# Optimization experiments

Measured on AMD Instinct MI355X. Metric: run time of the kernel, lower is better.

The kernel has to match this reference:

```python
import jax, jax.numpy as jnp
import numpy as np

BS, N, HID, INPUT, PREK, KHOP = 16, 1024, 64, 64, 4, 3
D = 2 * HID            # hidden channel dim (128)
F = 2 * INPUT          # input feature dim (128)
C = F + D              # graphconv input channels (256)
NM = KHOP + 1          # num_metrics = k_hop*n_supports + 1 with n_supports=1
PI = 3.141592653589793
EMB_RANGE = (12.0 + 2.0) / HID   # (gamma + epsilon) / hidden_size


def setup_inputs() -> dict:
    key = jax.random.key(0)
    ks = jax.random.split(key, 12)
    inputs = jax.random.normal(ks[0], (BS, N, F), jnp.float32)
    # per-sample dynamic support; scale by 1/N to keep Chebyshev recursion stable
    supports = jax.random.uniform(ks[1], (BS, N, N), jnp.float32) / N
    hidden_states = jax.random.normal(ks[2], (BS, PREK, N, D), jnp.float32)
    W = jax.random.normal(ks[3], (D, D), jnp.float32) * 0.02
    b = jax.random.normal(ks[4], (N, D), jnp.float32) * 0.02
    R = jax.random.normal(ks[5], (PREK, N, HID), jnp.float32) * 0.02
    gc_w = jax.random.normal(ks[6], (D, C * NM), jnp.float32) * 0.02
    gc_b = jax.random.normal(ks[7], (D,), jnp.float32) * 0.02
    ev_att_w = jax.random.normal(ks[8], (1, N * D), jnp.float32) * 0.001
    ev_att_b = jax.random.normal(ks[9], (1,), jnp.float32) * 0.02
    att_w = jax.random.normal(ks[10], (1, N * D), jnp.float32) * 0.001
    att_b = jax.random.normal(ks[11], (1,), jnp.float32) * 0.02
    return {"inputs": inputs, "supports": supports, "hidden_states": hidden_states,
            "W": W, "b": b, "R": R, "gc_w": gc_w, "gc_b": gc_b,
            "ev_att_w": ev_att_w, "ev_att_b": ev_att_b,
            "att_w": att_w, "att_b": att_b}


def reference(inputs, supports, hidden_states, W, b, R, gc_w, gc_b,
              ev_att_w, ev_att_b, att_w, att_b):
    bs, k, n, d = hidden_states.shape
    # split inputs / last hidden into real/imag halves
    re_in, im_in = jnp.split(inputs, 2, axis=-1)          # [bs,n,INPUT]
    preH = hidden_states[:, -1]                           # [bs,n,d]
    re_p, im_p = jnp.split(preH, 2, axis=-1)              # [bs,n,HID]
    conv_in = jnp.concatenate([re_in, re_p, im_in, im_p], axis=-1)  # [bs,n,C]

    # diffusion graph conv (Chebyshev-style recursion over single batched support)
    x0 = conv_in
    x1 = jnp.matmul(supports, x0)                         # [bs,n,C]
    xs = [x0, x1]
    for _ in range(2, KHOP + 1):
        x2 = 2.0 * jnp.matmul(supports, x1) - x0
        xs.append(x2)
        x0, x1 = x1, x2
    # stack K metrics, permute to [bs,n,C,K], flatten (channel-major, step-minor)
    x = jnp.stack(xs, axis=0).transpose(1, 2, 3, 0).reshape(bs, n, C * NM)
    gco = x @ gc_w.T + gc_b                               # [bs,n,d]

    # EvolutionCell attention over g=1 group (kept for faithfulness)
    xe = gco.reshape(bs, 1, n * d)
    se = xe @ ev_att_w.T + ev_att_b                       # [bs,1,1]
    we = jax.nn.softmax(se, axis=1)
    conv_out = (xe * we).sum(axis=1).reshape(bs, n, d)

    # leaky_relu_ (slope 0.01)
    conv_out = jnp.where(conv_out >= 0, conv_out, 0.01 * conv_out)

    # RotatE-style complex phase rotation of hidden states
    phase = R / (EMB_RANGE / PI)                          # [k,n,HID]
    re_rel, im_rel = jnp.cos(phase), jnp.sin(phase)
    re_h, im_h = jnp.split(hidden_states, 2, axis=-1)     # [bs,k,n,HID]
    re_new = re_rel * re_h - im_rel * im_h
    im_new = im_rel * re_h + re_rel * im_h
    new_states = jnp.concatenate([re_new, im_new], axis=-1)  # [bs,k,n,d]

    # attention over k memory slots
    xa = new_states.reshape(bs, k, n * d)
    sa = xa @ att_w.T + att_b                             # [bs,k,1]
    wa = jax.nn.softmax(sa, axis=1)
    att = (xa * wa).sum(axis=1).reshape(bs, n, d)

    output = conv_out @ W + b[None] + att                 # [bs,n,d]
    new_hidden = jnp.concatenate([hidden_states[:, 1:], output[:, None]], axis=1)
    return output, new_hidden
```

## Files before the change

### kernel.cpp

```cpp
#include <hip/hip_runtime.h>
#include <cstddef>

constexpr float PHASE_SCALE = (float)(3.141592653589793 / ((12.0 + 2.0) / 64.0));

typedef __bf16 bf16;
typedef __bf16 bf16x4 __attribute__((ext_vector_type(4)));
typedef __bf16 bf16x8 __attribute__((ext_vector_type(8)));
typedef float floatx4 __attribute__((ext_vector_type(4)));

__global__ __launch_bounds__(256) void prep_kernel(
    const float4* __restrict__ S, bf16* __restrict__ Sbf,
    const float* __restrict__ R,
    const float* __restrict__ gcw, const float* __restrict__ W,
    bf16* __restrict__ gtAll, bf16* __restrict__ WT,
    const float* __restrict__ inp, const float* __restrict__ hs,
    bf16* __restrict__ xAll, bf16* __restrict__ xT0,
    const float* __restrict__ attw, float* __restrict__ part)
{
    __shared__ bf16 tile[64][65];
    __shared__ float red[256];
    const int bid = blockIdx.x;
    const int tid = threadIdx.x;

    if (bid < 8192) {
        int gi = bid * 256 + tid;
        #pragma unroll
        for (int it = 0; it < 2; ++it) {
            int idx = gi + it * 2097152;
            float4 v = S[idx];
            bf16x4 o;
            o[0] = (bf16)v.x; o[1] = (bf16)v.y; o[2] = (bf16)v.z; o[3] = (bf16)v.w;
            *(bf16x4*)(Sbf + (size_t)idx * 4) = o;
        }
    } else if (bid < 9216) {
        int bid2 = bid - 8192;
        int b = bid2 >> 6;
        int by = (bid2 >> 2) & 15;
        int bx = bid2 & 3;
        int n0 = by * 64, c0 = bx * 64;
        #pragma unroll
        for (int it = 0; it < 16; ++it) {
            int idx = it * 256 + tid;
            int cl = idx & 63, nl = idx >> 6;
            int n = n0 + nl, c = c0 + cl;
            const float* irow = inp + ((size_t)b * 1024 + n) * 128;
            const float* prow = hs + (((size_t)b * 4 + 3) * 1024 + n) * 128;
            float v;
            if (c < 64)       v = irow[c];
            else if (c < 128) v = prow[c - 64];
            else if (c < 192) v = irow[c - 64];
            else              v = prow[c - 128];
            bf16 vb = (bf16)v;
            xAll[((size_t)b * 1024 + n) * 1024 + c] = vb;
            tile[nl][cl] = vb;
        }
        __syncthreads();
        #pragma unroll
        for (int it = 0; it < 16; ++it) {
            int idx = it * 256 + tid;
            int nl = idx & 63, cl = idx >> 6;
            xT0[((size_t)b * 256 + c0 + cl) * 1024 + n0 + nl] = tile[nl][cl];
        }
    } else if (bid < 9728) {
        int bid3 = bid - 9216;
        int bk = bid3 & 63;
        int k = bk & 3;
        int chunk = bid3 >> 6;
        const float* hbase = hs + (size_t)bk * 131072;
        float acc = 0.f;
        for (int idx = tid; idx < 2048; idx += 256) {
            int h4 = (idx & 15) * 4;
            int n = chunk * 128 + (idx >> 4);
            float4 rr  = *(const float4*)(R + (size_t)k * 65536 + n * 64 + h4);
            float4 re  = *(const float4*)(hbase + (size_t)n * 128 + h4);
            float4 im  = *(const float4*)(hbase + (size_t)n * 128 + 64 + h4);
            float4 wre = *(const float4*)(attw + (size_t)n * 128 + h4);
            float4 wim = *(const float4*)(attw + (size_t)n * 128 + 64 + h4);
            float sv, cv;
            __sincosf(rr.x * PHASE_SCALE, &sv, &cv);
            acc += (cv * re.x - sv * im.x) * wre.x + (sv * re.x + cv * im.x) * wim.x;
            __sincosf(rr.y * PHASE_SCALE, &sv, &cv);
            acc += (cv * re.y - sv * im.y) * wre.y + (sv * re.y + cv * im.y) * wim.y;
            __sincosf(rr.z * PHASE_SCALE, &sv, &cv);
            acc += (cv * re.z - sv * im.z) * wre.z + (sv * re.z + cv * im.z) * wim.z;
            __sincosf(rr.w * PHASE_SCALE, &sv, &cv);
            acc += (cv * re.w - sv * im.w) * wre.w + (sv * re.w + cv * im.w) * wim.w;
        }
        red[tid] = acc;
        __syncthreads();
        for (int s2 = 128; s2 > 0; s2 >>= 1) {
            if (tid < s2) red[tid] += red[tid + s2];
            __syncthreads();
        }
        if (tid == 0) part[bk * 8 + chunk] = red[0];
    } else {
        int gi = (bid - 9728) * 256 + tid;
        if (gi < 131072) {
            int d = gi >> 10;
            int m = (gi >> 8) & 3;
            int c = gi & 255;
            gtAll[gi] = (bf16)gcw[(size_t)d * 1024 + c * 4 + m];
        } else {
            int r = gi - 131072;
            int n = r >> 7, k = r & 127;
            WT[r] = (bf16)W[(size_t)k * 128 + n];
        }
    }
}

__global__ __launch_bounds__(256) void cheb_mfma_kernel(
    const bf16* __restrict__ S, const bf16* __restrict__ xT,
    const bf16* __restrict__ xTprev, bf16* __restrict__ outT,
    bf16* __restrict__ xAll, int mslot, float alpha)
{
    __shared__ bf16 ldsA[64 * 64];
    __shared__ bf16 ldsB[128 * 64];
    const int f = blockIdx.x;
    const int b = (f & 7) + 8 * ((f >> 3) & 1);
    const int t = f >> 4;
    const int c0 = (t & 1) * 128;
    const int n0 = (t >> 1) * 64;
    const int tid = threadIdx.x;
    const int wave = tid >> 6, lane = tid & 63;
    const int wr = (wave >> 1) * 32, wc = (wave & 1) * 64;
    const int l15 = lane & 15, quad = lane >> 4;

    const bf16* Sb = S + (size_t)b * 1048576;
    const bf16* xb = xT + (size_t)b * 262144;

    const int lrow = lane >> 3;
    const int segsw = (lane & 7) ^ lrow;

    floatx4 acc[2][4] = {};

    for (int k0 = 0; k0 < 1024; k0 += 64) {
        #pragma unroll
        for (int u = 0; u < 2; ++u) {
            int Rr = wave * 16 + u * 8;
            const bf16* gp = Sb + (size_t)(n0 + Rr + lrow) * 1024 + k0 + segsw * 8;
            __builtin_amdgcn_global_load_lds(
                (const __attribute__((address_space(1))) void*)gp,
                (__attribute__((address_space(3))) void*)(ldsA + Rr * 64), 16, 0, 0);
        }
        #pragma unroll
        for (int v = 0; v < 4; ++v) {
            int Cq = wave * 32 + v * 8;
            const bf16* gp = xb + (size_t)(c0 + Cq + lrow) * 1024 + k0 + segsw * 8;
            __builtin_amdgcn_global_load_lds(
                (const __attribute__((address_space(1))) void*)gp,
                (__attribute__((address_space(3))) void*)(ldsB + Cq * 64), 16, 0, 0);
        }
        __syncthreads();
        #pragma unroll
        for (int ks = 0; ks < 2; ++ks) {
            bf16x8 af[2], bfr[4];
            #pragma unroll
            for (int i = 0; i < 2; ++i) {
                int row = wr + i * 16 + l15;
                int slot = (ks * 4 + quad) ^ (row & 7);
                af[i] = *(const bf16x8*)(ldsA + row * 64 + slot * 8);
            }
            #pragma unroll
            for (int j = 0; j < 4; ++j) {
                int col = wc + j * 16 + l15;
                int slot = (ks * 4 + quad) ^ (col & 7);
                bfr[j] = *(const bf16x8*)(ldsB + col * 64 + slot * 8);
            }
            #pragma unroll
            for (int i = 0; i < 2; ++i)
                #pragma unroll
                for (int j = 0; j < 4; ++j)
                    acc[i][j] = __builtin_amdgcn_mfma_f32_16x16x32_bf16(af[i], bfr[j], acc[i][j], 0, 0, 0);
        }
        __syncthreads();
    }

    const bf16* pT = xTprev ? xTprev + (size_t)b * 262144 : nullptr;
    bf16* oT = outT ? outT + (size_t)b * 262144 : nullptr;
    bf16* xr = xAll + (size_t)b * 1048576 + mslot * 256;
    #pragma unroll
    for (int i = 0; i < 2; ++i) {
        int nb = n0 + wr + i * 16 + quad * 4;
        #pragma unroll
        for (int j = 0; j < 4; ++j) {
            int cg = c0 + wc + j * 16 + l15;
            float v[4];
            #pragma unroll
            for (int r = 0; r < 4; ++r) v[r] = alpha * acc[i][j][r];
            if (pT) {
                const bf16* pp = pT + (size_t)cg * 1024 + nb;
                #pragma unroll
                for (int r = 0; r < 4; ++r) v[r] -= (float)pp[r];
            }
            bf16x4 o;
            #pragma unroll
            for (int r = 0; r < 4; ++r) o[r] = (bf16)v[r];
            if (oT) *(bf16x4*)(oT + (size_t)cg * 1024 + nb) = o;
            #pragma unroll
            for (int r = 0; r < 4; ++r)
                xr[(size_t)(nb + r) * 1024 + cg] = o[r];
        }
    }
}

__global__ __launch_bounds__(256) void att_compute_copy_kernel(
    const float* __restrict__ hs, const float* __restrict__ R,
    const float* __restrict__ part, const float* __restrict__ attb,
    float* __restrict__ attB, float* __restrict__ newh)
{
    int gi = blockIdx.x * 256 + threadIdx.x;
    int d = gi & 127;
    int n = (gi >> 7) & 1023;
    int b = gi >> 17;
    int h = d & 63;
    bool isre = (d < 64);

    float sa[4], mx = -1e30f;
    #pragma unroll
    for (int k = 0; k < 4; ++k) {
        float s = attb[0];
        #pragma unroll
        for (int c = 0; c < 8; ++c) s += part[(b * 4 + k) * 8 + c];
        sa[k] = s;
        mx = fmaxf(mx, s);
    }
    float den = 0.f;
    #pragma unroll
    for (int k = 0; k < 4; ++k) { sa[k] = __expf(sa[k] - mx); den += sa[k]; }
    float inv = 1.f / den;

    float acc = 0.f;
    #pragma unroll
    for (int k = 0; k < 4; ++k) {
        float s, c;
        __sincosf(R[(size_t)k * 65536 + n * 64 + h] * PHASE_SCALE, &s, &c);
        const float* hb = hs + ((((size_t)b * 4 + k) * 1024 + n) * 128);
        float re = hb[h];
        float im = hb[64 + h];
        float v = isre ? (c * re - s * im) : (s * re + c * im);
        acc += (sa[k] * inv) * v;
        if (k >= 1)
            newh[(size_t)b * 524288 + (size_t)(k - 1) * 131072 + (size_t)n * 128 + d]
                = isre ? re : im;
    }
    attB[gi] = acc;
}

__global__ __launch_bounds__(256, 2) void gco_final_kernel(
    const bf16* __restrict__ xAll, const bf16* __restrict__ gtAll,
    const float* __restrict__ gcb, const bf16* __restrict__ WT,
    const float* __restrict__ bvec, const float* __restrict__ attB,
    float* __restrict__ out, float* __restrict__ newh)
{
    __shared__ bf16 ldsT[64 * 136];
    const int m0 = blockIdx.x * 64;
    const int tid = threadIdx.x;
    const int wave = tid >> 6, lane = tid & 63;
    const int l15 = lane & 15, quad = lane >> 4;

    const bf16* ap = xAll + (size_t)(m0 + wave * 16 + l15) * 1024 + quad * 8;
    const bf16* bp[8];
    #pragma unroll
    for (int j = 0; j < 8; ++j)
        bp[j] = gtAll + (size_t)(j * 16 + l15) * 1024 + quad * 8;

    floatx4 a1[8] = {};
    bf16x8 cA = *(const bf16x8*)ap;
    bf16x8 cB[8];
    #pragma unroll
    for (int j = 0; j < 8; ++j) cB[j] = *(const bf16x8*)(bp[j]);
    for (int k0 = 0; k0 < 992; k0 += 32) {
        bf16x8 nA = *(const bf16x8*)(ap + k0 + 32);
        bf16x8 nB[8];
        #pragma unroll
        for (int j = 0; j < 8; ++j) nB[j] = *(const bf16x8*)(bp[j] + k0 + 32);
        #pragma unroll
        for (int j = 0; j < 8; ++j)
            a1[j] = __builtin_amdgcn_mfma_f32_16x16x32_bf16(cA, cB[j], a1[j], 0, 0, 0);
        cA = nA;
        #pragma unroll
        for (int j = 0; j < 8; ++j) cB[j] = nB[j];
    }
    #pragma unroll
    for (int j = 0; j < 8; ++j)
        a1[j] = __builtin_amdgcn_mfma_f32_16x16x32_bf16(cA, cB[j], a1[j], 0, 0, 0);

    #pragma unroll
    for (int j = 0; j < 8; ++j) {
        int dcol = j * 16 + l15;
        float g = gcb[dcol];
        #pragma unroll
        for (int r = 0; r < 4; ++r) {
            int lrow = wave * 16 + quad * 4 + r;
            float v = a1[j][r] + g;
            v = v >= 0.f ? v : 0.01f * v;
            ldsT[lrow * 136 + dcol] = (bf16)v;
        }
    }
    __syncthreads();

    const bf16* wp[8];
    #pragma unroll
    for (int j = 0; j < 8; ++j)
        wp[j] = WT + (size_t)(j * 16 + l15) * 128 + quad * 8;
    const bf16* lp = ldsT + (wave * 16 + l15) * 136 + quad * 8;
    floatx4 a2[8] = {};
    #pragma unroll
    for (int k0 = 0; k0 < 128; k0 += 32) {
        bf16x8 af = *(const bf16x8*)(lp + k0);
        #pragma unroll
        for (int j = 0; j < 8; ++j) {
            bf16x8 bfr = *(const bf16x8*)(wp[j] + k0);
            a2[j] = __builtin_amdgcn_mfma_f32_16x16x32_bf16(af, bfr, a2[j], 0, 0, 0);
        }
    }
    #pragma unroll
    for (int j = 0; j < 8; ++j) {
        int col = j * 16 + l15;
        #pragma unroll
        for (int r = 0; r < 4; ++r) {
            int row = m0 + wave * 16 + quad * 4 + r;
            int bidx = row >> 10, n = row & 1023;
            float o = a2[j][r] + bvec[(size_t)n * 128 + col] + attB[(size_t)row * 128 + col];
            out[(size_t)row * 128 + col] = o;
            newh[(size_t)bidx * 524288 + 393216 + (size_t)n * 128 + col] = o;
        }
    }
}

extern "C" void kernel_launch(void* const* d_in, const int* in_sizes, int n_in,
                              void* d_out, int out_size, void* d_ws, size_t ws_size,
                              hipStream_t stream) {
    const float* inp  = (const float*)d_in[0];
    const float* sup  = (const float*)d_in[1];
    const float* hs   = (const float*)d_in[2];
    const float* W    = (const float*)d_in[3];
    const float* bvec = (const float*)d_in[4];
    const float* R    = (const float*)d_in[5];
    const float* gcw  = (const float*)d_in[6];
    const float* gcb  = (const float*)d_in[7];
    const float* attw = (const float*)d_in[10];
    const float* attb = (const float*)d_in[11];

    float* out  = (float*)d_out;
    float* newh = out + 2097152;
    bf16*  Sbf  = (bf16*)newh;

    char* w = (char*)d_ws;
    bf16*  xAll  = (bf16*)(w);
    bf16*  xTA   = (bf16*)(w + 33554432);
    bf16*  xTB   = (bf16*)(w + 41943040);
    bf16*  gtAll = (bf16*)(w + 50331648);
    bf16*  WT    = (bf16*)(w + 50593792);
    float* attB  = (float*)(w + 50626560);
    float* part  = (float*)(w + 59015168);

    prep_kernel<<<10304, 256, 0, stream>>>((const float4*)sup, Sbf, R, gcw, W,
                                           gtAll, WT, inp, hs, xAll, xTA, attw, part);

    cheb_mfma_kernel<<<512, 256, 0, stream>>>(Sbf, xTA, nullptr, xTB, xAll, 1, 1.0f);
    cheb_mfma_kernel<<<512, 256, 0, stream>>>(Sbf, xTB, xTA, xTA, xAll, 2, 2.0f);
    cheb_mfma_kernel<<<512, 256, 0, stream>>>(Sbf, xTA, xTB, nullptr, xAll, 3, 2.0f);

    att_compute_copy_kernel<<<8192, 256, 0, stream>>>(hs, R, part, attb, attB, newh);
    gco_final_kernel<<<256, 256, 0, stream>>>(xAll, gtAll, gcb, WT, bvec, attB, out, newh);
}
```

Baseline: 281.4 us.

## Fuse graphconv projection into Chebyshev kernels and merge attention into final kernel

Each Chebyshev step kernel now multiplies its freshly computed tile by the matching slice of the graphconv weight and accumulates into an fp32 gco buffer, so the large bf16 xAll concat buffer and the separate 1024-deep gco GEMM are gone. The Chebyshev kernel now uses 512 threads, covers all 256 channels per block, and double-buffers the LDS loads of S and x. The attention/rotation and newh copy kernel is folded into the final kernel alongside the W projection. The prep kernel reorders its sections and widens the S conversion to 8 elements per thread. The cost is read-modify-write of gcoF across three launches, more LDS per block, and fewer blocks for the Chebyshev GEMM.

```diff
diff --git a/kernel.cpp b/kernel.cpp
--- a/kernel.cpp
+++ b/kernel.cpp
@@ -7,6 +7,10 @@
 typedef __bf16 bf16x4 __attribute__((ext_vector_type(4)));
 typedef __bf16 bf16x8 __attribute__((ext_vector_type(8)));
 typedef float floatx4 __attribute__((ext_vector_type(4)));
+
+#define GLOAD_LDS16(gp, lp) __builtin_amdgcn_global_load_lds( \
+    (const __attribute__((address_space(1))) void*)(gp),      \
+    (__attribute__((address_space(3))) void*)(lp), 16, 0, 0)
 
 __global__ __launch_bounds__(256) void prep_kernel(
     const float4* __restrict__ S, bf16* __restrict__ Sbf,
@@ -14,7 +18,7 @@
     const float* __restrict__ gcw, const float* __restrict__ W,
     bf16* __restrict__ gtAll, bf16* __restrict__ WT,
     const float* __restrict__ inp, const float* __restrict__ hs,
-    bf16* __restrict__ xAll, bf16* __restrict__ xT0,
+    bf16* __restrict__ xRow, bf16* __restrict__ xT0,
     const float* __restrict__ attw, float* __restrict__ part)
 {
     __shared__ bf16 tile[64][65];
@@ -22,47 +26,21 @@
     const int bid = blockIdx.x;
     const int tid = threadIdx.x;
 
-    if (bid < 8192) {
+    if (bid < 576) {
         int gi = bid * 256 + tid;
-        #pragma unroll
-        for (int it = 0; it < 2; ++it) {
-            int idx = gi + it * 2097152;
-            float4 v = S[idx];
-            bf16x4 o;
-            o[0] = (bf16)v.x; o[1] = (bf16)v.y; o[2] = (bf16)v.z; o[3] = (bf16)v.w;
-            *(bf16x4*)(Sbf + (size_t)idx * 4) = o;
-        }
-    } else if (bid < 9216) {
-        int bid2 = bid - 8192;
-        int b = bid2 >> 6;
-        int by = (bid2 >> 2) & 15;
-        int bx = bid2 & 3;
-        int n0 = by * 64, c0 = bx * 64;
-        #pragma unroll
-        for (int it = 0; it < 16; ++it) {
-            int idx = it * 256 + tid;
-            int cl = idx & 63, nl = idx >> 6;
-            int n = n0 + nl, c = c0 + cl;
-            const float* irow = inp + ((size_t)b * 1024 + n) * 128;
-            const float* prow = hs + (((size_t)b * 4 + 3) * 1024 + n) * 128;
-            float v;
-            if (c < 64)       v = irow[c];
-            else if (c < 128) v = prow[c - 64];
-            else if (c < 192) v = irow[c - 64];
-            else              v = prow[c - 128];
-            bf16 vb = (bf16)v;
-            xAll[((size_t)b * 1024 + n) * 1024 + c] = vb;
-            tile[nl][cl] = vb;
-        }
-        __syncthreads();
-        #pragma unroll
-        for (int it = 0; it < 16; ++it) {
-            int idx = it * 256 + tid;
-            int nl = idx & 63, cl = idx >> 6;
-            xT0[((size_t)b * 256 + c0 + cl) * 1024 + n0 + nl] = tile[nl][cl];
-        }
-    } else if (bid < 9728) {
-        int bid3 = bid - 9216;
+        if (gi < 131072) {
+            int m = gi >> 15;
+            int rem = gi & 32767;
+            int d = rem >> 8;
+            int c = rem & 255;
+            gtAll[gi] = (bf16)gcw[(size_t)d * 1024 + c * 4 + m];
+        } else {
+            int r = gi - 131072;
+            int n = r >> 7, k = r & 127;
+            WT[r] = (bf16)W[(size_t)k * 128 + n];
+        }
+    } else if (bid < 1088) {
+        int bid3 = bid - 576;
         int bk = bid3 & 63;
         int k = bk & 3;
         int chunk = bid3 >> 6;
@@ -93,127 +71,208 @@
             __syncthreads();
         }
         if (tid == 0) part[bk * 8 + chunk] = red[0];
+    } else if (bid < 2112) {
+        int bid2 = bid - 1088;
+        int b = bid2 >> 6;
+        int by = (bid2 >> 2) & 15;
+        int bx = bid2 & 3;
+        int n0 = by * 64, c0 = bx * 64;
+        #pragma unroll
+        for (int it = 0; it < 16; ++it) {
+            int idx = it * 256 + tid;
+            int cl = idx & 63, nl = idx >> 6;
+            int n = n0 + nl, c = c0 + cl;
+            const float* irow = inp + ((size_t)b * 1024 + n) * 128;
+            const float* prow = hs + (((size_t)b * 4 + 3) * 1024 + n) * 128;
+            float v;
+            if (c < 64)       v = irow[c];
+            else if (c < 128) v = prow[c - 64];
+            else if (c < 192) v = irow[c - 64];
+            else              v = prow[c - 128];
+            bf16 vb = (bf16)v;
+            xRow[((size_t)b * 1024 + n) * 256 + c] = vb;
+            tile[nl][cl] = vb;
+        }
+        __syncthreads();
+        #pragma unroll
+        for (int it = 0; it < 16; ++it) {
+            int idx = it * 256 + tid;
+            int nl = idx & 63, cl = idx >> 6;
+            xT0[((size_t)b * 256 + c0 + cl) * 1024 + n0 + nl] = tile[nl][cl];
+        }
     } else {
-        int gi = (bid - 9728) * 256 + tid;
-        if (gi < 131072) {
-            int d = gi >> 10;
-            int m = (gi >> 8) & 3;
-            int c = gi & 255;
-            gtAll[gi] = (bf16)gcw[(size_t)d * 1024 + c * 4 + m];
-        } else {
-            int r = gi - 131072;
-            int n = r >> 7, k = r & 127;
-            WT[r] = (bf16)W[(size_t)k * 128 + n];
-        }
+        int gi = (bid - 2112) * 256 + tid;
+        const float4* Sp = S + (size_t)gi * 2;
+        float4 v0 = Sp[0];
+        float4 v1 = Sp[1];
+        bf16x8 o;
+        o[0] = (bf16)v0.x; o[1] = (bf16)v0.y; o[2] = (bf16)v0.z; o[3] = (bf16)v0.w;
+        o[4] = (bf16)v1.x; o[5] = (bf16)v1.y; o[6] = (bf16)v1.z; o[7] = (bf16)v1.w;
+        *(bf16x8*)(Sbf + (size_t)gi * 8) = o;
     }
 }
 
-__global__ __launch_bounds__(256) void cheb_mfma_kernel(
+__global__ __launch_bounds__(512) void cheb_mfma_kernel(
     const bf16* __restrict__ S, const bf16* __restrict__ xT,
     const bf16* __restrict__ xTprev, bf16* __restrict__ outT,
-    bf16* __restrict__ xAll, int mslot, float alpha)
+    const bf16* __restrict__ xRow0, const bf16* __restrict__ gtA,
+    const bf16* __restrict__ gt0, float* __restrict__ gcoF,
+    float alpha, int accumulate)
 {
-    __shared__ bf16 ldsA[64 * 64];
-    __shared__ bf16 ldsB[128 * 64];
+    __shared__ char smem[81920];
     const int f = blockIdx.x;
     const int b = (f & 7) + 8 * ((f >> 3) & 1);
-    const int t = f >> 4;
-    const int c0 = (t & 1) * 128;
-    const int n0 = (t >> 1) * 64;
+    const int n0 = (f >> 4) * 64;
     const int tid = threadIdx.x;
     const int wave = tid >> 6, lane = tid & 63;
-    const int wr = (wave >> 1) * 32, wc = (wave & 1) * 64;
+    const int wr = (wave & 3) * 16;
+    const int wc = (wave >> 2) * 128;
     const int l15 = lane & 15, quad = lane >> 4;
+    const int lrow = lane >> 3;
+    const int segsw = (lane & 7) ^ lrow;
 
     const bf16* Sb = S + (size_t)b * 1048576;
     const bf16* xb = xT + (size_t)b * 262144;
 
-    const int lrow = lane >> 3;
-    const int segsw = (lane & 7) ^ lrow;
-
-    floatx4 acc[2][4] = {};
-
+    auto stage = [&](int p, int k0) {
+        bf16* dA = (bf16*)(smem + p * 40960);
+        bf16* dB = dA + 4096;
+        {
+            const bf16* gp = Sb + (size_t)(n0 + wave * 8 + lrow) * 1024 + k0 + segsw * 8;
+            GLOAD_LDS16(gp, dA + wave * 8 * 64);
+        }
+        #pragma unroll
+        for (int v = 0; v < 4; ++v) {
+            int cq = wave * 32 + v * 8;
+            const bf16* gp = xb + (size_t)(cq + lrow) * 1024 + k0 + segsw * 8;
+            GLOAD_LDS16(gp, dB + cq * 64);
+        }
+    };
+
+    floatx4 acc[8] = {};
+    stage(0, 0);
+    int p = 0;
     for (int k0 = 0; k0 < 1024; k0 += 64) {
-        #pragma unroll
-        for (int u = 0; u < 2; ++u) {
-            int Rr = wave * 16 + u * 8;
-            const bf16* gp = Sb + (size_t)(n0 + Rr + lrow) * 1024 + k0 + segsw * 8;
-            __builtin_amdgcn_global_load_lds(
-                (const __attribute__((address_space(1))) void*)gp,
-                (__attribute__((address_space(3))) void*)(ldsA + Rr * 64), 16, 0, 0);
-        }
-        #pragma unroll
-        for (int v = 0; v < 4; ++v) {
-            int Cq = wave * 32 + v * 8;
-            const bf16* gp = xb + (size_t)(c0 + Cq + lrow) * 1024 + k0 + segsw * 8;
-            __builtin_amdgcn_global_load_lds(
-                (const __attribute__((address_space(1))) void*)gp,
-                (__attribute__((address_space(3))) void*)(ldsB + Cq * 64), 16, 0, 0);
-        }
         __syncthreads();
+        if (k0 + 64 < 1024) stage(p ^ 1, k0 + 64);
+        const bf16* lA = (const bf16*)(smem + p * 40960);
+        const bf16* lB = lA + 4096;
         #pragma unroll
         for (int ks = 0; ks < 2; ++ks) {
-            bf16x8 af[2], bfr[4];
+            int row = wr + l15;
+            int aslot = (ks * 4 + quad) ^ (row & 7);
+            bf16x8 af = *(const bf16x8*)(lA + row * 64 + aslot * 8);
             #pragma unroll
-            for (int i = 0; i < 2; ++i) {
-                int row = wr + i * 16 + l15;
-                int slot = (ks * 4 + quad) ^ (row & 7);
-                af[i] = *(const bf16x8*)(ldsA + row * 64 + slot * 8);
+            for (int j = 0; j < 8; ++j) {
+                int col = wc + j * 16 + l15;
+                int bslot = (ks * 4 + quad) ^ (col & 7);
+                bf16x8 bfr = *(const bf16x8*)(lB + col * 64 + bslot * 8);
+                acc[j] = __builtin_amdgcn_mfma_f32_16x16x32_bf16(af, bfr, acc[j], 0, 0, 0);
             }
+        }
+        p ^= 1;
+    }
+
+    const bf16* pT = xTprev ? xTprev + (size_t)b * 262144 : nullptr;
+    bf16* oT = outT ? outT + (size_t)b * 262144 : nullptr;
+    bf16x4 xo[8];
+    #pragma unroll
+    for (int j = 0; j < 8; ++j) {
+        int col = wc + j * 16 + l15;
+        float v[4];
+        #pragma unroll
+        for (int r = 0; r < 4; ++r) v[r] = alpha * acc[j][r];
+        if (pT) {
+            bf16x4 pp = *(const bf16x4*)(pT + (size_t)col * 1024 + n0 + wr + quad * 4);
+            #pragma unroll
+            for (int r = 0; r < 4; ++r) v[r] -= (float)pp[r];
+        }
+        #pragma unroll
+        for (int r = 0; r < 4; ++r) xo[j][r] = (bf16)v[r];
+        if (oT) *(bf16x4*)(oT + (size_t)col * 1024 + n0 + wr + quad * 4) = xo[j];
+    }
+
+    __syncthreads();
+    bf16* ldsX = (bf16*)smem;
+    #pragma unroll
+    for (int j = 0; j < 8; ++j) {
+        int col = wc + j * 16 + l15;
+        #pragma unroll
+        for (int r = 0; r < 4; ++r)
+            ldsX[(wr + quad * 4 + r) * 264 + col] = xo[j][r];
+    }
+    __syncthreads();
+
+    const int dbase = (wave >> 2) * 64;
+    floatx4 a2[4] = {};
+    for (int k2 = 0; k2 < 256; k2 += 32) {
+        bf16x8 af = *(const bf16x8*)(ldsX + (wr + l15) * 264 + k2 + quad * 8);
+        #pragma unroll
+        for (int j = 0; j < 4; ++j) {
+            int dcol = dbase + j * 16 + l15;
+            bf16x8 bfr = *(const bf16x8*)(gtA + (size_t)dcol * 256 + k2 + quad * 8);
+            a2[j] = __builtin_amdgcn_mfma_f32_16x16x32_bf16(af, bfr, a2[j], 0, 0, 0);
+        }
+    }
+    if (xRow0) {
+        for (int k2 = 0; k2 < 256; k2 += 32) {
+            bf16x8 af = *(const bf16x8*)(xRow0 + ((size_t)b * 1024 + n0 + wr + l15) * 256 + k2 + quad * 8);
             #pragma unroll
             for (int j = 0; j < 4; ++j) {
-                int col = wc + j * 16 + l15;
-                int slot = (ks * 4 + quad) ^ (col & 7);
-                bfr[j] = *(const bf16x8*)(ldsB + col * 64 + slot * 8);
+                int dcol = dbase + j * 16 + l15;
+                bf16x8 bfr = *(const bf16x8*)(gt0 + (size_t)dcol * 256 + k2 + quad * 8);
+                a2[j] = __builtin_amdgcn_mfma_f32_16x16x32_bf16(af, bfr, a2[j], 0, 0, 0);
             }
-            #pragma unroll
-            for (int i = 0; i < 2; ++i)
-                #pragma unroll
-                for (int j = 0; j < 4; ++j)
-                    acc[i][j] = __builtin_amdgcn_mfma_f32_16x16x32_bf16(af[i], bfr[j], acc[i][j], 0, 0, 0);
-        }
-        __syncthreads();
-    }
-
-    const bf16* pT = xTprev ? xTprev + (size_t)b * 262144 : nullptr;
-    bf16* oT = outT ? outT + (size_t)b * 262144 : nullptr;
-    bf16* xr = xAll + (size_t)b * 1048576 + mslot * 256;
-    #pragma unroll
-    for (int i = 0; i < 2; ++i) {
-        int nb = n0 + wr + i * 16 + quad * 4;
-        #pragma unroll
-        for (int j = 0; j < 4; ++j) {
-            int cg = c0 + wc + j * 16 + l15;
-            float v[4];
-            #pragma unroll
-            for (int r = 0; r < 4; ++r) v[r] = alpha * acc[i][j][r];
-            if (pT) {
-                const bf16* pp = pT + (size_t)cg * 1024 + nb;
-                #pragma unroll
-                for (int r = 0; r < 4; ++r) v[r] -= (float)pp[r];
-            }
-            bf16x4 o;
-            #pragma unroll
-            for (int r = 0; r < 4; ++r) o[r] = (bf16)v[r];
-            if (oT) *(bf16x4*)(oT + (size_t)cg * 1024 + nb) = o;
-            #pragma unroll
-            for (int r = 0; r < 4; ++r)
-                xr[(size_t)(nb + r) * 1024 + cg] = o[r];
+        }
+    }
+    #pragma unroll
+    for (int j = 0; j < 4; ++j) {
+        int dcol = dbase + j * 16 + l15;
+        #pragma unroll
+        for (int r = 0; r < 4; ++r) {
+            size_t idx = ((size_t)b * 1024 + n0 + wr + quad * 4 + r) * 128 + dcol;
+            if (accumulate) gcoF[idx] += a2[j][r];
+            else            gcoF[idx]  = a2[j][r];
         }
     }
 }
 
-__global__ __launch_bounds__(256) void att_compute_copy_kernel(
+__global__ __launch_bounds__(256) void final_kernel(
+    const float* __restrict__ gcoF, const float* __restrict__ gcb,
+    const bf16* __restrict__ WT, const float* __restrict__ bvec,
     const float* __restrict__ hs, const float* __restrict__ R,
     const float* __restrict__ part, const float* __restrict__ attb,
-    float* __restrict__ attB, float* __restrict__ newh)
+    float* __restrict__ out, float* __restrict__ newh)
 {
-    int gi = blockIdx.x * 256 + threadIdx.x;
-    int d = gi & 127;
-    int n = (gi >> 7) & 1023;
-    int b = gi >> 17;
-    int h = d & 63;
-    bool isre = (d < 64);
+    const int m0 = blockIdx.x * 64;
+    const int b = m0 >> 10, n0 = m0 & 1023;
+    const int tid = threadIdx.x;
+    const int wave = tid >> 6, lane = tid & 63;
+    const int l15 = lane & 15, quad = lane >> 4;
+
+    const int arow = m0 + wave * 16 + l15;
+    floatx4 acc[8] = {};
+    #pragma unroll
+    for (int k0 = 0; k0 < 128; k0 += 32) {
+        int kk = k0 + quad * 8;
+        float4 p0 = *(const float4*)(gcoF + (size_t)arow * 128 + kk);
+        float4 p1 = *(const float4*)(gcoF + (size_t)arow * 128 + kk + 4);
+        float4 g0 = *(const float4*)(gcb + kk);
+        float4 g1 = *(const float4*)(gcb + kk + 4);
+        float vv[8] = {p0.x + g0.x, p0.y + g0.y, p0.z + g0.z, p0.w + g0.w,
+                       p1.x + g1.x, p1.y + g1.y, p1.z + g1.z, p1.w + g1.w};
+        bf16x8 af;
+        #pragma unroll
+        for (int e = 0; e < 8; ++e) {
+            float v = vv[e];
+            af[e] = (bf16)(v >= 0.f ? v : 0.01f * v);
+        }
+        #pragma unroll
+        for (int j = 0; j < 8; ++j) {
+            bf16x8 bfr = *(const bf16x8*)(WT + (size_t)(j * 16 + l15) * 128 + kk);
+            acc[j] = __builtin_amdgcn_mfma_f32_16x16x32_bf16(af, bfr, acc[j], 0, 0, 0);
+        }
+    }
 
     float sa[4], mx = -1e30f;
     #pragma unroll
@@ -228,102 +287,38 @@
     #pragma unroll
     for (int k = 0; k < 4; ++k) { sa[k] = __expf(sa[k] - mx); den += sa[k]; }
     float inv = 1.f / den;
-
-    float acc = 0.f;
-    #pragma unroll
-    for (int k = 0; k < 4; ++k) {
-        float s, c;
-        __sincosf(R[(size_t)k * 65536 + n * 64 + h] * PHASE_SCALE, &s, &c);
-        const float* hb = hs + ((((size_t)b * 4 + k) * 1024 + n) * 128);
-        float re = hb[h];
-        float im = hb[64 + h];
-        float v = isre ? (c * re - s * im) : (s * re + c * im);
-        acc += (sa[k] * inv) * v;
-        if (k >= 1)
-            newh[(size_t)b * 524288 + (size_t)(k - 1) * 131072 + (size_t)n * 128 + d]
-                = isre ? re : im;
-    }
-    attB[gi] = acc;
-}
-
-__global__ __launch_bounds__(256, 2) void gco_final_kernel(
-    const bf16* __restrict__ xAll, const bf16* __restrict__ gtAll,
-    const float* __restrict__ gcb, const bf16* __restrict__ WT,
-    const float* __restrict__ bvec, const float* __restrict__ attB,
-    float* __restrict__ out, float* __restrict__ newh)
-{
-    __shared__ bf16 ldsT[64 * 136];
-    const int m0 = blockIdx.x * 64;
-    const int tid = threadIdx.x;
-    const int wave = tid >> 6, lane = tid & 63;
-    const int l15 = lane & 15, quad = lane >> 4;
-
-    const bf16* ap = xAll + (size_t)(m0 + wave * 16 + l15) * 1024 + quad * 8;
-    const bf16* bp[8];
-    #pragma unroll
-    for (int j = 0; j < 8; ++j)
-        bp[j] = gtAll + (size_t)(j * 16 + l15) * 1024 + quad * 8;
-
-    floatx4 a1[8] = {};
-    bf16x8 cA = *(const bf16x8*)ap;
-    bf16x8 cB[8];
-    #pragma unroll
-    for (int j = 0; j < 8; ++j) cB[j] = *(const bf16x8*)(bp[j]);
-    for (int k0 = 0; k0 < 992; k0 += 32) {
-        bf16x8 nA = *(const bf16x8*)(ap + k0 + 32);
-        bf16x8 nB[8];
-        #pragma unroll
-        for (int j = 0; j < 8; ++j) nB[j] = *(const bf16x8*)(bp[j] + k0 + 32);
-        #pragma unroll
-        for (int j = 0; j < 8; ++j)
-            a1[j] = __builtin_amdgcn_mfma_f32_16x16x32_bf16(cA, cB[j], a1[j], 0, 0, 0);
-        cA = nA;
-        #pragma unroll
-        for (int j = 0; j < 8; ++j) cB[j] = nB[j];
-    }
-    #pragma unroll
-    for (int j = 0; j < 8; ++j)
-        a1[j] = __builtin_amdgcn_mfma_f32_16x16x32_bf16(cA, cB[j], a1[j], 0, 0, 0);
-
-    #pragma unroll
-    for (int j = 0; j < 8; ++j) {
-        int dcol = j * 16 + l15;
-        float g = gcb[dcol];
+    #pragma unroll
+    for (int k = 0; k < 4; ++k) sa[k] *= inv;
+
+    #pragma unroll
+    for (int jj = 0; jj < 4; ++jj) {
+        int hcol = jj * 16 + l15;
         #pragma unroll
         for (int r = 0; r < 4; ++r) {
-            int lrow = wave * 16 + quad * 4 + r;
-            float v = a1[j][r] + g;
-            v = v >= 0.f ? v : 0.01f * v;
-            ldsT[lrow * 136 + dcol] = (bf16)v;
-        }
-    }
-    __syncthreads();
-
-    const bf16* wp[8];
-    #pragma unroll
-    for (int j = 0; j < 8; ++j)
-        wp[j] = WT + (size_t)(j * 16 + l15) * 128 + quad * 8;
-    const bf16* lp = ldsT + (wave * 16 + l15) * 136 + quad * 8;
-    floatx4 a2[8] = {};
-    #pragma unroll
-    for (int k0 = 0; k0 < 128; k0 += 32) {
-        bf16x8 af = *(const bf16x8*)(lp + k0);
-        #pragma unroll
-        for (int j = 0; j < 8; ++j) {
-            bf16x8 bfr = *(const bf16x8*)(wp[j] + k0);
-            a2[j] = __builtin_amdgcn_mfma_f32_16x16x32_bf16(af, bfr, a2[j], 0, 0, 0);
-        }
-    }
-    #pragma unroll
-    for (int j = 0; j < 8; ++j) {
-        int col = j * 16 + l15;
-        #pragma unroll
-        for (int r = 0; r < 4; ++r) {
-            int row = m0 + wave * 16 + quad * 4 + r;
-            int bidx = row >> 10, n = row & 1023;
-            float o = a2[j][r] + bvec[(size_t)n * 128 + col] + attB[(size_t)row * 128 + col];
-            out[(size_t)row * 128 + col] = o;
-            newh[(size_t)bidx * 524288 + 393216 + (size_t)n * 128 + col] = o;
+            int n = n0 + wave * 16 + quad * 4 + r;
+            float attRe = 0.f, attIm = 0.f;
+            #pragma unroll
+            for (int k = 0; k < 4; ++k) {
+                const float* hb = hs + (((size_t)(b * 4 + k) * 1024 + n) * 128);
+                float re = hb[hcol], im = hb[64 + hcol];
+                float s, c;
+                __sincosf(R[(size_t)k * 65536 + n * 64 + hcol] * PHASE_SCALE, &s, &c);
+                attRe += sa[k] * (c * re - s * im);
+                attIm += sa[k] * (s * re + c * im);
+                if (k >= 1) {
+                    size_t nb = (size_t)b * 524288 + (size_t)(k - 1) * 131072 + (size_t)n * 128;
+                    newh[nb + hcol] = re;
+                    newh[nb + 64 + hcol] = im;
+                }
+            }
+            size_t ob = (size_t)(m0 + wave * 16 + quad * 4 + r) * 128;
+            float oRe = acc[jj][r]     + bvec[(size_t)n * 128 + hcol]      + attRe;
+            float oIm = acc[jj + 4][r] + bvec[(size_t)n * 128 + 64 + hcol] + attIm;
+            out[ob + hcol] = oRe;
+            out[ob + 64 + hcol] = oIm;
+            size_t nb3 = (size_t)b * 524288 + 393216 + (size_t)n * 128;
+            newh[nb3 + hcol] = oRe;
+            newh[nb3 + 64 + hcol] = oIm;
         }
     }
 }
@@ -347,21 +342,24 @@
     bf16*  Sbf  = (bf16*)newh;
 
     char* w = (char*)d_ws;
-    bf16*  xAll  = (bf16*)(w);
-    bf16*  xTA   = (bf16*)(w + 33554432);
-    bf16*  xTB   = (bf16*)(w + 41943040);
-    bf16*  gtAll = (bf16*)(w + 50331648);
-    bf16*  WT    = (bf16*)(w + 50593792);
-    float* attB  = (float*)(w + 50626560);
-    float* part  = (float*)(w + 59015168);
+    bf16*  xT0   = (bf16*)(w);
+    bf16*  xT1   = (bf16*)(w + 8388608);
+    bf16*  xT2   = (bf16*)(w + 16777216);
+    bf16*  xRow  = (bf16*)(w + 25165824);
+    float* gcoF  = (float*)(w + 33554432);
+    bf16*  gtAll = (bf16*)(w + 41943040);
+    bf16*  WT    = (bf16*)(w + 42205184);
+    float* part  = (float*)(w + 42237952);
 
     prep_kernel<<<10304, 256, 0, stream>>>((const float4*)sup, Sbf, R, gcw, W,
-                                           gtAll, WT, inp, hs, xAll, xTA, attw, part);
-
-    cheb_mfma_kernel<<<512, 256, 0, stream>>>(Sbf, xTA, nullptr, xTB, xAll, 1, 1.0f);
-    cheb_mfma_kernel<<<512, 256, 0, stream>>>(Sbf, xTB, xTA, xTA, xAll, 2, 2.0f);
-    cheb_mfma_kernel<<<512, 256, 0, stream>>>(Sbf, xTA, xTB, nullptr, xAll, 3, 2.0f);
-
-    att_compute_copy_kernel<<<8192, 256, 0, stream>>>(hs, R, part, attb, attB, newh);
-    gco_final_kernel<<<256, 256, 0, stream>>>(xAll, gtAll, gcb, WT, bvec, attB, out, newh);
+                                           gtAll, WT, inp, hs, xRow, xT0, attw, part);
+
+    cheb_mfma_kernel<<<256, 512, 0, stream>>>(Sbf, xT0, nullptr, xT1,
+                                              xRow, gtAll + 32768, gtAll, gcoF, 1.0f, 0);
+    cheb_mfma_kernel<<<256, 512, 0, stream>>>(Sbf, xT1, xT0, xT2,
+                                              nullptr, gtAll + 2 * 32768, nullptr, gcoF, 2.0f, 1);
+    cheb_mfma_kernel<<<256, 512, 0, stream>>>(Sbf, xT2, xT1, nullptr,
+                                              nullptr, gtAll + 3 * 32768, nullptr, gcoF, 2.0f, 1);
+
+    final_kernel<<<256, 256, 0, stream>>>(gcoF, gcb, WT, bvec, hs, R, part, attb, out, newh);
 }
```

Result: faster. 265.0 us (-5.8%).
